# Optimization experiments

Measured on AMD Instinct MI355X. Metric: run time of the kernel, lower is better.

## Reference

```python
import jax, jax.numpy as jnp
import numpy as np

PATCH, STRIDE, NUM_PROJ, NBINS = 7, 1, 16, 2 ** 16
B, C, H, W = 2, 3, 384, 384


def gaussian_kernel(size=7, sigma=1.2):
    x = jnp.arange(size, dtype=jnp.float32)
    # faithful to original: exp(...)**2 (square applied OUTSIDE the exp)
    return jnp.exp((x - size // 2) ** 2 / (-2.0 * sigma ** 2)) ** 2


def extract_patches(img, p, s):
    # Equivalent of F.unfold: [b, c, h, w] -> [b, N, c*p*p], torch channel-major feature order
    b, c, h, w = img.shape
    Ho = (h - p) // s + 1
    Wo = (w - p) // s + 1
    cols = [img[:, :, i:i + (Ho - 1) * s + 1:s, j:j + (Wo - 1) * s + 1:s]
            for i in range(p) for j in range(p)]
    pat = jnp.stack(cols, axis=2)  # [b, c, p*p, Ho, Wo]
    return pat.reshape(b, c * p * p, Ho * Wo).transpose(0, 2, 1)  # [b, N, c*p*p]


def hist_distance(px, py):
    # px, py: [N] projected values for one (batch, projection) pair
    min_v = jnp.minimum(py.min(), px.min())
    max_v = jnp.maximum(py.max(), px.max())
    scale = max_v - min_v
    # scatter-set 1s into a 65536-bin histogram at data-dependent indices
    y_idx = jnp.floor((NBINS - 1) * (py - min_v) / scale).astype(jnp.int32)
    y_hist = jnp.zeros((NBINS,), jnp.float32).at[y_idx].set(1.0)
    # valid conv1d with 7-tap gaussian (symmetric kernel, so corr == conv)
    y_hist = jnp.convolve(y_hist, gaussian_kernel(), mode='valid')  # [NBINS-6]
    y_hist = jnp.minimum(y_hist, 1.0)
    Wd = y_hist.shape[0]
    # grid_sample (bilinear, align_corners=False, zero padding) on a 1-tall image == 1D linear interp
    gx = 2.0 * (px - min_v) / scale - 1.0
    ix = ((gx + 1.0) * Wd - 1.0) / 2.0
    x0 = jnp.floor(ix)
    w1 = ix - x0
    x0i = x0.astype(jnp.int32)
    x1i = x0i + 1
    v0 = jnp.where((x0i >= 0) & (x0i < Wd), y_hist[jnp.clip(x0i, 0, Wd - 1)], 0.0)
    v1 = jnp.where((x1i >= 0) & (x1i < Wd), y_hist[jnp.clip(x1i, 0, Wd - 1)], 0.0)
    return -(v0 * (1.0 - w1) + v1 * w1).sum()


def setup_inputs() -> dict:
    key = jax.random.key(0)
    k1, k2, k3 = jax.random.split(key, 3)
    x = jax.random.normal(k1, (B, C, H, W), dtype=jnp.float32)
    y = jax.random.normal(k2, (B, C, H, W), dtype=jnp.float32)
    rand = jax.random.normal(k3, (B, C * PATCH * PATCH, NUM_PROJ), dtype=jnp.float32)
    return {"x": x, "y": y, "rand": rand}


def reference(x, y, rand):
    xp = extract_patches(x, PATCH, STRIDE)  # [b, N, d]
    yp = extract_patches(y, PATCH, STRIDE)
    # torch.std(dim=0) is unbiased (ddof=1)
    r = rand / jnp.std(rand, axis=1, keepdims=True, ddof=1)  # [b, d, P]
    proj_x = jnp.einsum('bnd,bdp->bpn', xp, r)
    proj_y = jnp.einsum('bnd,bdp->bpn', yp, r)
    losses = jax.vmap(jax.vmap(hist_distance))(proj_x, proj_y)  # [b, P]
    per_image = losses.sum(axis=1) / NUM_PROJ
    return per_image.mean()  # batch_reduction='mean'
```

## Files before the change

kernel.cpp:

```cpp
#include <hip/hip_runtime.h>
#include <math.h>
#include <stdint.h>

#define NPROJ 16
#define NBINS 65536
#define WD (NBINS - 6)
#define BMW 2056
#define B_ 2
#define C_ 3
#define H_ 384
#define W_ 384
#define HO 378
#define NPAT (HO * HO)
#define DF 147
#define BP 32

__device__ inline unsigned f2key(float f) {
    unsigned u = __float_as_uint(f);
    return (u & 0x80000000u) ? ~u : (u | 0x80000000u);
}
__device__ inline float key2f(unsigned k) {
    unsigned u = (k & 0x80000000u) ? (k ^ 0x80000000u) : ~k;
    return __uint_as_float(u);
}

__global__ __launch_bounds__(64) void k_rnorm(const float* __restrict__ rnd,
                                              float* __restrict__ rnorm,
                                              unsigned* __restrict__ keys,
                                              unsigned* __restrict__ bitmap,
                                              float* __restrict__ out) {
    int bp = blockIdx.x;
    int b = bp / NPROJ, p = bp % NPROJ;
    int lane = threadIdx.x;
    if (lane == 0) {
        keys[2 * bp] = 0xFFFFFFFFu;
        keys[2 * bp + 1] = 0u;
        if (bp == 0) out[0] = 0.f;
    }
    for (int i = bp * 64 + lane; i < BP * BMW; i += BP * 64)
        bitmap[i] = 0u;

    float s = 0.f, s2 = 0.f;
    for (int d = lane; d < DF; d += 64) {
        float v = rnd[((size_t)b * DF + d) * NPROJ + p];
        s += v; s2 += v * v;
    }
    for (int o = 32; o > 0; o >>= 1) { s += __shfl_down(s, o); s2 += __shfl_down(s2, o); }
    s = __shfl(s, 0); s2 = __shfl(s2, 0);
    float mean = s / (float)DF;
    float var = (s2 - (float)DF * mean * mean) / (float)(DF - 1);
    float inv = 1.0f / sqrtf(var);
    for (int d = lane; d < DF; d += 64) {
        size_t idx = ((size_t)b * DF + d) * NPROJ + p;
        rnorm[idx] = rnd[idx] * inv;
    }
}

#define TW 32
#define TH 16
#define TSTR2 40
__global__ __launch_bounds__(256) void k_projmm(const float* __restrict__ ximg,
                                                const float* __restrict__ yimg,
                                                const float* __restrict__ rnorm,
                                                float* __restrict__ px,
                                                float* __restrict__ py,
                                                unsigned* __restrict__ keys) {
    __shared__ float tile[C_][TH + 6][TSTR2];
    __shared__ float red_mn[4][NPROJ], red_mx[4][NPROJ];
    int bz = blockIdx.z;
    int b = bz >> 1, isy = bz & 1;
    const float* img = isy ? yimg : ximg;
    float* proj = isy ? py : px;
    int tid = threadIdx.x;
    int tx = tid & 15, ty = tid >> 4;
    int h0 = blockIdx.y * TH, w0 = blockIdx.x * TW;

    for (int c = 0; c < C_; c++)
        for (int i = tid; i < (TH + 6) * (TW + 6); i += 256) {
            int r = i / (TW + 6), col = i % (TW + 6);
            int h = h0 + r, w = w0 + col;
            tile[c][r][col] = (h < H_ && w < W_)
                ? img[((size_t)(b * C_ + c) * H_ + h) * W_ + w] : 0.f;
        }
    __syncthreads();

    const float* wbase = rnorm + (size_t)b * DF * NPROJ;

    float acc[2][NPROJ];
#pragma unroll
    for (int q = 0; q < 2; q++)
#pragma unroll
        for (int p = 0; p < NPROJ; p++) acc[q][p] = 0.f;

    for (int c = 0; c < C_; c++)
        for (int i = 0; i < 7; i++) {
            float pxr[8];
            const float2* row = (const float2*)&tile[c][ty + i][2 * tx];
#pragma unroll
            for (int q = 0; q < 4; q++) {
                float2 t2 = row[q];
                pxr[2 * q] = t2.x; pxr[2 * q + 1] = t2.y;
            }
#pragma unroll
            for (int j = 0; j < 7; j++) {
                const float* wrow = wbase + (c * 49 + i * 7 + j) * NPROJ;
                float wv[NPROJ];
#pragma unroll
                for (int p = 0; p < NPROJ; p++) wv[p] = wrow[p];
#pragma unroll
                for (int p = 0; p < NPROJ; p++) {
                    acc[0][p] = fmaf(pxr[j], wv[p], acc[0][p]);
                    acc[1][p] = fmaf(pxr[j + 1], wv[p], acc[1][p]);
                }
            }
        }

    int wo = w0 + 2 * tx;
    int ho = h0 + ty;
    bool vm = (ho < HO) && (wo < HO);

    if (vm) {
        size_t n = (size_t)ho * HO + wo;
#pragma unroll
        for (int p = 0; p < NPROJ; p++)
            *(float2*)&proj[((size_t)(b * NPROJ + p)) * NPAT + n] =
                make_float2(acc[0][p], acc[1][p]);
    }

    float pmn[NPROJ], pmx[NPROJ];
#pragma unroll
    for (int p = 0; p < NPROJ; p++) {
        float mn = INFINITY, mx = -INFINITY;
        if (vm) {
            mn = fminf(acc[0][p], acc[1][p]);
            mx = fmaxf(acc[0][p], acc[1][p]);
        }
        pmn[p] = mn; pmx[p] = mx;
    }
#pragma unroll
    for (int o = 1; o < 64; o <<= 1) {
#pragma unroll
        for (int p = 0; p < NPROJ; p++) {
            pmn[p] = fminf(pmn[p], __shfl_xor(pmn[p], o));
            pmx[p] = fmaxf(pmx[p], __shfl_xor(pmx[p], o));
        }
    }
    int wv4 = tid >> 6;
    if ((tid & 63) == 0) {
#pragma unroll
        for (int p = 0; p < NPROJ; p++) { red_mn[wv4][p] = pmn[p]; red_mx[wv4][p] = pmx[p]; }
    }
    __syncthreads();
    if (tid < NPROJ) {
        float mn = fminf(fminf(red_mn[0][tid], red_mn[1][tid]),
                         fminf(red_mn[2][tid], red_mn[3][tid]));
        float mx = fmaxf(fmaxf(red_mx[0][tid], red_mx[1][tid]),
                         fmaxf(red_mx[2][tid], red_mx[3][tid]));
        atomicMin(&keys[2 * (b * NPROJ + tid)], f2key(mn));
        atomicMax(&keys[2 * (b * NPROJ + tid) + 1], f2key(mx));
    }
}

__global__ __launch_bounds__(256) void k_scatter(const float* __restrict__ py,
                                                 const unsigned* __restrict__ keys,
                                                 unsigned* __restrict__ bitmap) {
    __shared__ unsigned lbm[BMW];
    int bp = blockIdx.y;
    int tid = threadIdx.x;
    for (int i = tid; i < BMW; i += 256) lbm[i] = 0u;
    __syncthreads();

    float mn = key2f(keys[2 * bp]);
    float sc = key2f(keys[2 * bp + 1]) - mn;
    const float4* src = (const float4*)(py + (size_t)bp * NPAT);
    const int n4 = NPAT / 4;
    for (int i = blockIdx.x * blockDim.x + tid; i < n4;
         i += gridDim.x * blockDim.x) {
        float4 v = src[i];
        float vv[4] = { v.x, v.y, v.z, v.w };
#pragma unroll
        for (int j = 0; j < 4; j++) {
            int idx = (int)floorf(65535.f * (vv[j] - mn) / sc);
            int bit = 8 + min(max(idx, 0), 65535);
            atomicOr(&lbm[bit >> 5], 1u << (bit & 31));
        }
    }
    __syncthreads();
    unsigned* dst = bitmap + (size_t)bp * BMW;
    for (int i = tid; i < BMW; i += 256) {
        unsigned w = lbm[i];
        if (w) atomicOr(&dst[i], w);
    }
}

__global__ __launch_bounds__(256) void k_gather(const float* __restrict__ px,
                                                const unsigned* __restrict__ keys,
                                                const unsigned* __restrict__ bitmap,
                                                float* __restrict__ out) {
    __shared__ unsigned lbm[BMW];
    __shared__ float2 lut[256];
    __shared__ float sred[4];
    int bp = blockIdx.y;
    int tid = threadIdx.x;

    const unsigned* gbm = bitmap + (size_t)bp * BMW;
    for (int i = tid; i < BMW; i += 256) lbm[i] = gbm[i];

    float g[7];
#pragma unroll
    for (int k = 0; k < 7; k++) {
        float d = (float)(k - 3);
        g[k] = expf(-(d * d) / 1.44f);
    }
    {
        int m = tid;
        float f[8];
#pragma unroll
        for (int k = 0; k < 8; k++) f[k] = (float)((m >> k) & 1);
        float s0 = g[0] * f[0] + g[1] * f[1] + g[2] * f[2] + g[3] * f[3]
                 + g[4] * f[4] + g[5] * f[5] + g[6] * f[6];
        float s1 = g[0] * f[1] + g[1] * f[2] + g[2] * f[3] + g[3] * f[4]
                 + g[4] * f[5] + g[5] * f[6] + g[6] * f[7];
        lut[m] = make_float2(fminf(s0, 1.f), fminf(s1, 1.f));
    }
    __syncthreads();

    float mn = key2f(keys[2 * bp]);
    float sc = key2f(keys[2 * bp + 1]) - mn;
    const float4* src = (const float4*)(px + (size_t)bp * NPAT);

    float acc = 0.f;
    const int n4 = NPAT / 4;
    for (int i = blockIdx.x * blockDim.x + tid; i < n4;
         i += gridDim.x * blockDim.x) {
        float4 v4 = src[i];
        float vv[4] = { v4.x, v4.y, v4.z, v4.w };
#pragma unroll
        for (int j = 0; j < 4; j++) {
            float v = vv[j];
            float t = (v - mn) / sc;
            float ix = t * (float)WD - 0.5f;
            float x0 = floorf(ix);
            float w1 = ix - x0;
            int x0i = (int)x0;
            int bit0 = 8 + x0i;
            int w = bit0 >> 5, s = bit0 & 31;
            uint64_t d = (uint64_t)lbm[w] | ((uint64_t)lbm[w + 1] << 32);
            uint32_t w8 = (uint32_t)(d >> s) & 0xFFu;
            float2 sv = lut[w8];
            float r0 = (x0i >= 0) ? sv.x : 0.f;
            float r1 = (x0i + 1 < WD) ? sv.y : 0.f;
            acc += r0 * (1.f - w1) + r1 * w1;
        }
    }
    for (int o = 32; o > 0; o >>= 1) acc += __shfl_down(acc, o);
    int wv4 = tid >> 6;
    if ((tid & 63) == 0) sred[wv4] = acc;
    __syncthreads();
    if (tid == 0) {
        float t = sred[0] + sred[1] + sred[2] + sred[3];
        atomicAdd(out, -t * (1.0f / 32.0f));
    }
}

extern "C" void kernel_launch(void* const* d_in, const int* in_sizes, int n_in,
                              void* d_out, int out_size, void* d_ws, size_t ws_size,
                              hipStream_t stream) {
    (void)in_sizes; (void)n_in; (void)out_size; (void)ws_size;
    const float* x = (const float*)d_in[0];
    const float* y = (const float*)d_in[1];
    const float* rnd = (const float*)d_in[2];
    float* out = (float*)d_out;

    float* ws = (float*)d_ws;
    float* rnorm = ws;
    float* px = rnorm + (size_t)B_ * DF * NPROJ;
    float* py = px + (size_t)BP * NPAT;
    unsigned* keys = (unsigned*)(py + (size_t)BP * NPAT);
    unsigned* bitmap = keys + 2 * BP;

    k_rnorm<<<BP, 64, 0, stream>>>(rnd, rnorm, keys, bitmap, out);

    dim3 g1(384 / TW, 384 / TH, 2 * B_);
    k_projmm<<<g1, 256, 0, stream>>>(x, y, rnorm, px, py, keys);

    k_scatter<<<dim3(16, BP), 256, 0, stream>>>(py, keys, bitmap);
    k_gather<<<dim3(70, BP), 256, 0, stream>>>(px, keys, bitmap, out);
}
```

Baseline: 105.1 us.

## Replace LDS bitmap atomics with global byte-histogram plain stores

The scatter kernel stops building a per-block LDS bitmap with atomicOr and merging it into global memory. It now writes a byte flag per bin directly to a global 64K-byte histogram with plain stores, which are idempotent and need no atomics. The gather kernel packs those bytes back into a bitmap in LDS using bit tricks, and the grid sizes of both kernels change. The cost is 32x more histogram memory to zero and read (about 2 MB), plus scattered byte writes to global memory.

After: 108.3 us. 1.03x slower.

```diff
diff --git a/kernel.cpp b/kernel.cpp
--- a/kernel.cpp
+++ b/kernel.cpp
@@ -5,6 +5,7 @@
 #define NPROJ 16
 #define NBINS 65536
 #define WD (NBINS - 6)
+#define HB 65792
 #define BMW 2056
 #define B_ 2
 #define C_ 3
@@ -27,7 +28,7 @@
 __global__ __launch_bounds__(64) void k_rnorm(const float* __restrict__ rnd,
                                               float* __restrict__ rnorm,
                                               unsigned* __restrict__ keys,
-                                              unsigned* __restrict__ bitmap,
+                                              uint4* __restrict__ hist16,
                                               float* __restrict__ out) {
     int bp = blockIdx.x;
     int b = bp / NPROJ, p = bp % NPROJ;
@@ -37,8 +38,10 @@
         keys[2 * bp + 1] = 0u;
         if (bp == 0) out[0] = 0.f;
     }
-    for (int i = bp * 64 + lane; i < BP * BMW; i += BP * 64)
-        bitmap[i] = 0u;
+    const int HW16 = BP * HB / 16;
+    uint4 z = make_uint4(0u, 0u, 0u, 0u);
+    for (int i = bp * 64 + lane; i < HW16; i += BP * 64)
+        hist16[i] = z;
 
     float s = 0.f, s2 = 0.f;
     for (int d = lane; d < DF; d += 64) {
@@ -163,39 +166,30 @@
 
 __global__ __launch_bounds__(256) void k_scatter(const float* __restrict__ py,
                                                  const unsigned* __restrict__ keys,
-                                                 unsigned* __restrict__ bitmap) {
-    __shared__ unsigned lbm[BMW];
+                                                 uint8_t* __restrict__ hist8) {
     int bp = blockIdx.y;
-    int tid = threadIdx.x;
-    for (int i = tid; i < BMW; i += 256) lbm[i] = 0u;
-    __syncthreads();
-
     float mn = key2f(keys[2 * bp]);
     float sc = key2f(keys[2 * bp + 1]) - mn;
     const float4* src = (const float4*)(py + (size_t)bp * NPAT);
+    uint8_t* h = hist8 + (size_t)bp * HB + 8;
     const int n4 = NPAT / 4;
-    for (int i = blockIdx.x * blockDim.x + tid; i < n4;
+    for (int i = blockIdx.x * blockDim.x + threadIdx.x; i < n4;
          i += gridDim.x * blockDim.x) {
         float4 v = src[i];
-        float vv[4] = { v.x, v.y, v.z, v.w };
-#pragma unroll
-        for (int j = 0; j < 4; j++) {
-            int idx = (int)floorf(65535.f * (vv[j] - mn) / sc);
-            int bit = 8 + min(max(idx, 0), 65535);
-            atomicOr(&lbm[bit >> 5], 1u << (bit & 31));
-        }
-    }
-    __syncthreads();
-    unsigned* dst = bitmap + (size_t)bp * BMW;
-    for (int i = tid; i < BMW; i += 256) {
-        unsigned w = lbm[i];
-        if (w) atomicOr(&dst[i], w);
+        int i0 = (int)floorf(65535.f * (v.x - mn) / sc);
+        int i1 = (int)floorf(65535.f * (v.y - mn) / sc);
+        int i2 = (int)floorf(65535.f * (v.z - mn) / sc);
+        int i3 = (int)floorf(65535.f * (v.w - mn) / sc);
+        h[min(max(i0, 0), 65535)] = 1;
+        h[min(max(i1, 0), 65535)] = 1;
+        h[min(max(i2, 0), 65535)] = 1;
+        h[min(max(i3, 0), 65535)] = 1;
     }
 }
 
 __global__ __launch_bounds__(256) void k_gather(const float* __restrict__ px,
                                                 const unsigned* __restrict__ keys,
-                                                const unsigned* __restrict__ bitmap,
+                                                const uint8_t* __restrict__ hist8,
                                                 float* __restrict__ out) {
     __shared__ unsigned lbm[BMW];
     __shared__ float2 lut[256];
@@ -203,8 +197,18 @@
     int bp = blockIdx.y;
     int tid = threadIdx.x;
 
-    const unsigned* gbm = bitmap + (size_t)bp * BMW;
-    for (int i = tid; i < BMW; i += 256) lbm[i] = gbm[i];
+    const uint4* src16 = (const uint4*)(hist8 + (size_t)bp * HB);
+    for (int d = tid; d < BMW; d += 256) {
+        uint4 a = src16[2 * d], b = src16[2 * d + 1];
+        uint32_t u[8] = { a.x, a.y, a.z, a.w, b.x, b.y, b.z, b.w };
+        uint32_t w = 0;
+#pragma unroll
+        for (int k = 0; k < 8; k++) {
+            uint32_t nib = (u[k] | (u[k] >> 7) | (u[k] >> 14) | (u[k] >> 21)) & 0xFu;
+            w |= nib << (4 * k);
+        }
+        lbm[d] = w;
+    }
 
     float g[7];
 #pragma unroll
@@ -277,13 +281,13 @@
     float* px = rnorm + (size_t)B_ * DF * NPROJ;
     float* py = px + (size_t)BP * NPAT;
     unsigned* keys = (unsigned*)(py + (size_t)BP * NPAT);
-    unsigned* bitmap = keys + 2 * BP;
-
-    k_rnorm<<<BP, 64, 0, stream>>>(rnd, rnorm, keys, bitmap, out);
+    uint8_t* hist8 = (uint8_t*)(keys + 2 * BP);
+
+    k_rnorm<<<BP, 64, 0, stream>>>(rnd, rnorm, keys, (uint4*)hist8, out);
 
     dim3 g1(384 / TW, 384 / TH, 2 * B_);
     k_projmm<<<g1, 256, 0, stream>>>(x, y, rnorm, px, py, keys);
 
-    k_scatter<<<dim3(16, BP), 256, 0, stream>>>(py, keys, bitmap);
-    k_gather<<<dim3(70, BP), 256, 0, stream>>>(px, keys, bitmap, out);
-}
+    k_scatter<<<dim3(70, BP), 256, 0, stream>>>(py, keys, hist8);
+    k_gather<<<dim3(35, BP), 256, 0, stream>>>(px, keys, hist8, out);
+}
```
